# Kernel tuning notes

Hardware: AMD Instinct MI355X
Metric: run time of the kernel (lower is better)

The kernel has to match this reference:

```python
import jax, jax.numpy as jnp
import numpy as np

THRESHOLD = 0.5
ALPHA = 1.0
N, D = 100000, 256
B, K = 1024, 128


def _l2norm(x):
    # F.normalize(x, p=2, dim=-1) with eps=1e-12
    return x / jnp.maximum(jnp.linalg.norm(x, axis=-1, keepdims=True), 1e-12)


def setup_inputs() -> dict:
    key = jax.random.key(0)
    k1, k2, k3, k4, k5, k6, k7 = jax.random.split(key, 7)
    feature = jax.random.normal(k1, (N, D), dtype=jnp.float32)
    text_embedding = jax.random.normal(k2, (N, D), dtype=jnp.float32)
    virtual = jax.random.normal(k3, (1, D), dtype=jnp.float32)
    # Gumbel(0,1) noise for gumbel_softmax (tau=1), materialized for determinism
    u = jax.random.uniform(k4, (B, K, K), dtype=jnp.float32, minval=1e-6, maxval=1.0 - 1e-6)
    gumbel = -jnp.log(-jnp.log(u))
    ego_nodes = jnp.sort(jax.random.randint(k5, (B, K), 0, N, dtype=jnp.int32), axis=-1)
    edges_adj = jax.random.randint(k6, (B, K, K), 0, 2, dtype=jnp.int32)
    train_label = jax.random.randint(k7, (B,), 0, 2, dtype=jnp.int32)
    return {"feature": feature, "text_embedding": text_embedding, "virtual": virtual,
            "gumbel": gumbel, "ego_nodes": ego_nodes, "edges_adj": edges_adj,
            "train_label": train_label}


def reference(feature, text_embedding, virtual, gumbel, ego_nodes, edges_adj, train_label):
    feat = _l2norm(feature)          # self.feature (normalized in __init__)
    emb = _l2norm(text_embedding)    # self.embedding
    te_local = _l2norm(emb - virtual)            # [N, D]

    tb = te_local[ego_nodes]                     # [B, K, D] gather per ego-subgraph
    sim = jnp.einsum('bkd,bjd->bkj', tb, tb) - THRESHOLD   # [B, K, K]
    sim_sub = jax.nn.softmax(sim + gumbel, axis=-1)         # gumbel_softmax, tau=1

    adj = edges_adj.astype(sim_sub.dtype)        # scatter edges_adj[src,dst]=1, precomputed
    # s_diff: row-wise L2 norm then mean over rows
    s_diff = jnp.sqrt(jnp.sum((adj - sim_sub) ** 2, axis=-1)).mean(axis=-1)   # [B]

    emb_out = feat[ego_nodes].mean(axis=1)       # [B, D] sum(feature)/n
    emb_pg = emb[ego_nodes].mean(axis=1)         # [B, D] sum(embedding)/n  (n == K)
    f_diff = jnp.linalg.norm(emb_out - emb_pg, axis=-1)                        # [B]

    score = s_diff + ALPHA * f_diff
    score = (score - score.min()) / (score.max() - score.min())

    y = train_label.astype(score.dtype)
    eps = 1e-7  # stabilizes log at exact 0/1 (torch BCELoss clamps log at -100)
    sc = jnp.clip(score, eps, 1.0 - eps)
    bce = -(y * jnp.log(sc) + (1.0 - y) * jnp.log1p(-sc)).mean()
    loss = bce / y.shape[0]
    return score, loss
```

## Files before the change

kernel.cpp:

```cpp
#include <hip/hip_runtime.h>
#include <math.h>

#define DIM 256
#define BB 1024
#define KK 128
#define PITCH 264

typedef __attribute__((ext_vector_type(8))) short short8;
typedef __attribute__((ext_vector_type(4))) float float4v;

__device__ __forceinline__ unsigned short f2bf(float x) {
    unsigned u = __float_as_uint(x);
    u += 0x7FFFu + ((u >> 16) & 1u);
    return (unsigned short)(u >> 16);
}

__device__ __forceinline__ float dot4(const float4 a, const float4 b) {
    return a.x*b.x + a.y*b.y + a.z*b.z + a.w*b.w;
}

__global__ __launch_bounds__(512, 4) void fused_main(
    const float* __restrict__ feature,
    const float* __restrict__ text,
    const float* __restrict__ virt,
    const float* __restrict__ gumbel,
    const int*   __restrict__ ego,
    const int*   __restrict__ adj,
    float*       __restrict__ score_raw)
{
    __shared__ unsigned short tbs[KK * PITCH];
    __shared__ float fpart[8][DIM];
    __shared__ float spart[8];

    const int b    = blockIdx.x;
    const int tid  = threadIdx.x;
    const int wave = tid >> 6;
    const int lane = tid & 63;

    const float4 vv = ((const float4*)virt)[lane];
    float vv2 = dot4(vv, vv);
    #pragma unroll
    for (int m = 1; m < 64; m <<= 1) vv2 += __shfl_xor(vv2, m);

    const int* ego_b = ego + b * KK;
    const int  base  = wave * 16;

    float fd0 = 0.f, fd1 = 0.f, fd2 = 0.f, fd3 = 0.f;

    int ea = ego_b[base + 0], eb = ego_b[base + 1];
    float4 nta = ((const float4*)(text    + (size_t)ea * DIM))[lane];
    float4 nfa = ((const float4*)(feature + (size_t)ea * DIM))[lane];
    float4 ntb = ((const float4*)(text    + (size_t)eb * DIM))[lane];
    float4 nfb = ((const float4*)(feature + (size_t)eb * DIM))[lane];

    #pragma unroll
    for (int kk = 0; kk < 16; kk += 2) {
        const float4 at = nta, af = nfa, bt = ntb, bf = nfb;
        if (kk + 2 < 16) {
            const int na = ego_b[base + kk + 2], nb = ego_b[base + kk + 3];
            nta = ((const float4*)(text    + (size_t)na * DIM))[lane];
            nfa = ((const float4*)(feature + (size_t)na * DIM))[lane];
            ntb = ((const float4*)(text    + (size_t)nb * DIM))[lane];
            nfb = ((const float4*)(feature + (size_t)nb * DIM))[lane];
        }
        float sta = dot4(at, at), sfa = dot4(af, af), sva = dot4(at, vv);
        float stb = dot4(bt, bt), sfb = dot4(bf, bf), svb = dot4(bt, vv);
        #pragma unroll
        for (int m = 1; m < 64; m <<= 1) {
            sta += __shfl_xor(sta, m);  sfa += __shfl_xor(sfa, m);  sva += __shfl_xor(sva, m);
            stb += __shfl_xor(stb, m);  sfb += __shfl_xor(sfb, m);  svb += __shfl_xor(svb, m);
        }
        {
            const float inv_ne = 1.f / fmaxf(sqrtf(sta), 1e-12f);
            const float inv_nf = 1.f / fmaxf(sqrtf(sfa), 1e-12f);
            const float nw2    = fmaxf(1.f + vv2 - 2.f * sva * inv_ne, 0.f);
            const float inv_nt = 1.f / fmaxf(sqrtf(nw2), 1e-12f);
            const float ex = at.x*inv_ne, ey = at.y*inv_ne, ez = at.z*inv_ne, ew = at.w*inv_ne;
            fd0 += af.x*inv_nf - ex;  fd1 += af.y*inv_nf - ey;
            fd2 += af.z*inv_nf - ez;  fd3 += af.w*inv_nf - ew;
            ushort4 pk;
            pk.x = f2bf((ex - vv.x) * inv_nt);
            pk.y = f2bf((ey - vv.y) * inv_nt);
            pk.z = f2bf((ez - vv.z) * inv_nt);
            pk.w = f2bf((ew - vv.w) * inv_nt);
            *(ushort4*)&tbs[(base + kk) * PITCH + 4 * lane] = pk;
        }
        {
            const float inv_ne = 1.f / fmaxf(sqrtf(stb), 1e-12f);
            const float inv_nf = 1.f / fmaxf(sqrtf(sfb), 1e-12f);
            const float nw2    = fmaxf(1.f + vv2 - 2.f * svb * inv_ne, 0.f);
            const float inv_nt = 1.f / fmaxf(sqrtf(nw2), 1e-12f);
            const float ex = bt.x*inv_ne, ey = bt.y*inv_ne, ez = bt.z*inv_ne, ew = bt.w*inv_ne;
            fd0 += bf.x*inv_nf - ex;  fd1 += bf.y*inv_nf - ey;
            fd2 += bf.z*inv_nf - ez;  fd3 += bf.w*inv_nf - ew;
            ushort4 pk;
            pk.x = f2bf((ex - vv.x) * inv_nt);
            pk.y = f2bf((ey - vv.y) * inv_nt);
            pk.z = f2bf((ez - vv.z) * inv_nt);
            pk.w = f2bf((ew - vv.w) * inv_nt);
            *(ushort4*)&tbs[(base + kk + 1) * PITCH + 4 * lane] = pk;
        }
    }
    fpart[wave][4*lane + 0] = fd0;
    fpart[wave][4*lane + 1] = fd1;
    fpart[wave][4*lane + 2] = fd2;
    fpart[wave][4*lane + 3] = fd3;
    __syncthreads();

    const int g = lane >> 4;
    const int c = lane & 15;

    const float* gb = gumbel + (size_t)b * KK * KK;
    const int*   ab = adj    + (size_t)b * KK * KK;

    float gvv[32];
    #pragma unroll
    for (int r = 0; r < 4; ++r) {
        const float* gr = gb + (base + g*4 + r) * KK + c;
        #pragma unroll
        for (int t = 0; t < 8; ++t)
            gvv[r*8 + t] = __builtin_nontemporal_load(gr + t*16);
    }

    float4v acc[8];
    const float4v zero = {0.f, 0.f, 0.f, 0.f};
    #pragma unroll
    for (int t = 0; t < 8; ++t) acc[t] = zero;

    #pragma unroll
    for (int q = 0; q < 8; ++q) {
        const int dq = q * 32 + g * 8;
        const short8 afr = *(const short8*)&tbs[(base + c) * PITCH + dq];
        #pragma unroll
        for (int t = 0; t < 8; ++t) {
            const short8 bfr = *(const short8*)&tbs[(t*16 + c) * PITCH + dq];
            acc[t] = __builtin_amdgcn_mfma_f32_16x16x32_bf16(afr, bfr, acc[t], 0, 0, 0);
        }
    }

    int avv[32];
    #pragma unroll
    for (int r = 0; r < 4; ++r) {
        const int* ar = ab + (base + g*4 + r) * KK + c;
        #pragma unroll
        for (int t = 0; t < 8; ++t)
            avv[r*8 + t] = __builtin_nontemporal_load(ar + t*16);
    }

    float rs = 0.f;
    #pragma unroll
    for (int r = 0; r < 4; ++r) {
        float s = 0.f, a1 = 0.f, a2 = 0.f, a3 = 0.f;
        #pragma unroll
        for (int t = 0; t < 8; ++t) {
            const float vt = acc[t][r] - 0.5f + gvv[r*8 + t];
            const float et = __expf(vt);
            const float ad = (float)avv[r*8 + t];
            s  += et;
            a3 += et * et;
            a1 += ad;
            a2 += ad * et;
        }
        #pragma unroll
        for (int msk = 1; msk < 16; msk <<= 1) {
            s  += __shfl_xor(s,  msk);
            a1 += __shfl_xor(a1, msk);
            a2 += __shfl_xor(a2, msk);
            a3 += __shfl_xor(a3, msk);
        }
        const float invS = 1.f / s;
        const float T = a1 - 2.f * invS * a2 + invS * invS * a3;
        rs += sqrtf(fmaxf(T, 0.f));
    }
    rs += __shfl_xor(rs, 16);
    rs += __shfl_xor(rs, 32);
    if (lane == 0) spart[wave] = rs;
    __syncthreads();

    if (wave == 0) {
        float d0 = 0.f, d1 = 0.f, d2 = 0.f, d3 = 0.f;
        #pragma unroll
        for (int w = 0; w < 8; ++w) {
            d0 += fpart[w][lane];
            d1 += fpart[w][lane + 64];
            d2 += fpart[w][lane + 128];
            d3 += fpart[w][lane + 192];
        }
        const float inv = 1.f / 128.f;
        d0 *= inv; d1 *= inv; d2 *= inv; d3 *= inv;
        float q2 = d0*d0 + d1*d1 + d2*d2 + d3*d3;
        #pragma unroll
        for (int m = 1; m < 64; m <<= 1) q2 += __shfl_xor(q2, m);
        if (lane == 0) {
            float stot = 0.f;
            #pragma unroll
            for (int w = 0; w < 8; ++w) stot += spart[w];
            score_raw[b] = stot * (1.f / 128.f) + sqrtf(q2);
        }
    }
}

__global__ __launch_bounds__(1024) void finalize(
    const float* __restrict__ score_raw,
    const int*   __restrict__ label,
    float*       __restrict__ out)
{
    __shared__ float wmin[16], wmax[16], wsum[16];
    const int tid = threadIdx.x;
    const float s = score_raw[tid];
    float mn = s, mx = s;
    #pragma unroll
    for (int m = 1; m < 64; m <<= 1) {
        mn = fminf(mn, __shfl_xor(mn, m));
        mx = fmaxf(mx, __shfl_xor(mx, m));
    }
    if ((tid & 63) == 0) { wmin[tid >> 6] = mn; wmax[tid >> 6] = mx; }
    __syncthreads();
    float gmn = wmin[0], gmx = wmax[0];
    #pragma unroll
    for (int w = 1; w < 16; ++w) {
        gmn = fminf(gmn, wmin[w]);
        gmx = fmaxf(gmx, wmax[w]);
    }
    const float score = (s - gmn) / (gmx - gmn);
    out[tid] = score;

    const float y  = (float)label[tid];
    const float sc = fminf(fmaxf(score, 1e-7f), 1.f - 1e-7f);
    float term = -(y * logf(sc) + (1.f - y) * log1pf(-sc));
    #pragma unroll
    for (int m = 1; m < 64; m <<= 1) term += __shfl_xor(term, m);
    if ((tid & 63) == 0) wsum[tid >> 6] = term;
    __syncthreads();
    if (tid == 0) {
        float tot = 0.f;
        #pragma unroll
        for (int w = 0; w < 16; ++w) tot += wsum[w];
        out[BB] = tot / (1024.f * 1024.f);
    }
}

extern "C" void kernel_launch(void* const* d_in, const int* in_sizes, int n_in,
                              void* d_out, int out_size, void* d_ws, size_t ws_size,
                              hipStream_t stream) {
    const float* feature = (const float*)d_in[0];
    const float* text    = (const float*)d_in[1];
    const float* virt    = (const float*)d_in[2];
    const float* gumbel  = (const float*)d_in[3];
    const int*   ego     = (const int*)d_in[4];
    const int*   adj     = (const int*)d_in[5];
    const int*   label   = (const int*)d_in[6];
    float* out       = (float*)d_out;
    float* score_raw = (float*)d_ws;

    fused_main<<<BB, 512, 0, stream>>>(feature, text, virt, gumbel, ego, adj, score_raw);
    finalize<<<1, 1024, 0, stream>>>(score_raw, label, out);
}
```

Measured before the change: 76.09 us.

## Remap gather phase to 16-lane row groups and move gumbel load ahead of barrier

The normalization/gather phase now assigns each quarter-wave (16 lanes) to one node row, with each lane holding 16 floats. This replaces full-wave 64-lane shuffle reductions with 16-lane reductions, processing 4 rows in parallel per iteration. It also uses hardware rsq/rcp intrinsics and packed bf16 conversion, and issues the gumbel loads before the barrier so they overlap the barrier wait. In exchange, register pressure rises and the approximate rsq/rcp may differ slightly in precision from the exact division and sqrt.

```diff
diff --git a/kernel.cpp b/kernel.cpp
--- a/kernel.cpp
+++ b/kernel.cpp
@@ -1,4 +1,5 @@
 #include <hip/hip_runtime.h>
+#include <hip/hip_bf16.h>
 #include <math.h>
 
 #define DIM 256
@@ -9,14 +10,15 @@
 typedef __attribute__((ext_vector_type(8))) short short8;
 typedef __attribute__((ext_vector_type(4))) float float4v;
 
-__device__ __forceinline__ unsigned short f2bf(float x) {
-    unsigned u = __float_as_uint(x);
-    u += 0x7FFFu + ((u >> 16) & 1u);
-    return (unsigned short)(u >> 16);
-}
-
 __device__ __forceinline__ float dot4(const float4 a, const float4 b) {
     return a.x*b.x + a.y*b.y + a.z*b.z + a.w*b.w;
+}
+
+__device__ __forceinline__ unsigned bf2bits(float a, float b) {
+    float2 t; t.x = a; t.y = b;
+    __hip_bfloat162 h = __float22bfloat162_rn(t);
+    unsigned u; __builtin_memcpy(&u, &h, 4);
+    return u;
 }
 
 __global__ __launch_bounds__(512, 4) void fused_main(
@@ -36,83 +38,110 @@
     const int tid  = threadIdx.x;
     const int wave = tid >> 6;
     const int lane = tid & 63;
-
-    const float4 vv = ((const float4*)virt)[lane];
-    float vv2 = dot4(vv, vv);
-    #pragma unroll
-    for (int m = 1; m < 64; m <<= 1) vv2 += __shfl_xor(vv2, m);
+    const int g    = lane >> 4;
+    const int c    = lane & 15;
+
+    float4 vm[4];
+    #pragma unroll
+    for (int m = 0; m < 4; ++m) vm[m] = *(const float4*)(virt + 64*m + 4*c);
+
+    float vv2 = 0.f;
+    #pragma unroll
+    for (int m = 0; m < 4; ++m) vv2 += dot4(vm[m], vm[m]);
+    #pragma unroll
+    for (int msk = 1; msk < 16; msk <<= 1) vv2 += __shfl_xor(vv2, msk);
 
     const int* ego_b = ego + b * KK;
     const int  base  = wave * 16;
 
-    float fd0 = 0.f, fd1 = 0.f, fd2 = 0.f, fd3 = 0.f;
-
-    int ea = ego_b[base + 0], eb = ego_b[base + 1];
-    float4 nta = ((const float4*)(text    + (size_t)ea * DIM))[lane];
-    float4 nfa = ((const float4*)(feature + (size_t)ea * DIM))[lane];
-    float4 ntb = ((const float4*)(text    + (size_t)eb * DIM))[lane];
-    float4 nfb = ((const float4*)(feature + (size_t)eb * DIM))[lane];
-
-    #pragma unroll
-    for (int kk = 0; kk < 16; kk += 2) {
-        const float4 at = nta, af = nfa, bt = ntb, bf = nfb;
-        if (kk + 2 < 16) {
-            const int na = ego_b[base + kk + 2], nb = ego_b[base + kk + 3];
-            nta = ((const float4*)(text    + (size_t)na * DIM))[lane];
-            nfa = ((const float4*)(feature + (size_t)na * DIM))[lane];
-            ntb = ((const float4*)(text    + (size_t)nb * DIM))[lane];
-            nfb = ((const float4*)(feature + (size_t)nb * DIM))[lane];
-        }
-        float sta = dot4(at, at), sfa = dot4(af, af), sva = dot4(at, vv);
-        float stb = dot4(bt, bt), sfb = dot4(bf, bf), svb = dot4(bt, vv);
-        #pragma unroll
-        for (int m = 1; m < 64; m <<= 1) {
-            sta += __shfl_xor(sta, m);  sfa += __shfl_xor(sfa, m);  sva += __shfl_xor(sva, m);
-            stb += __shfl_xor(stb, m);  sfb += __shfl_xor(sfb, m);  svb += __shfl_xor(svb, m);
-        }
-        {
-            const float inv_ne = 1.f / fmaxf(sqrtf(sta), 1e-12f);
-            const float inv_nf = 1.f / fmaxf(sqrtf(sfa), 1e-12f);
-            const float nw2    = fmaxf(1.f + vv2 - 2.f * sva * inv_ne, 0.f);
-            const float inv_nt = 1.f / fmaxf(sqrtf(nw2), 1e-12f);
-            const float ex = at.x*inv_ne, ey = at.y*inv_ne, ez = at.z*inv_ne, ew = at.w*inv_ne;
-            fd0 += af.x*inv_nf - ex;  fd1 += af.y*inv_nf - ey;
-            fd2 += af.z*inv_nf - ez;  fd3 += af.w*inv_nf - ew;
-            ushort4 pk;
-            pk.x = f2bf((ex - vv.x) * inv_nt);
-            pk.y = f2bf((ey - vv.y) * inv_nt);
-            pk.z = f2bf((ez - vv.z) * inv_nt);
-            pk.w = f2bf((ew - vv.w) * inv_nt);
-            *(ushort4*)&tbs[(base + kk) * PITCH + 4 * lane] = pk;
-        }
-        {
-            const float inv_ne = 1.f / fmaxf(sqrtf(stb), 1e-12f);
-            const float inv_nf = 1.f / fmaxf(sqrtf(sfb), 1e-12f);
-            const float nw2    = fmaxf(1.f + vv2 - 2.f * svb * inv_ne, 0.f);
-            const float inv_nt = 1.f / fmaxf(sqrtf(nw2), 1e-12f);
-            const float ex = bt.x*inv_ne, ey = bt.y*inv_ne, ez = bt.z*inv_ne, ew = bt.w*inv_ne;
-            fd0 += bf.x*inv_nf - ex;  fd1 += bf.y*inv_nf - ey;
-            fd2 += bf.z*inv_nf - ez;  fd3 += bf.w*inv_nf - ew;
-            ushort4 pk;
-            pk.x = f2bf((ex - vv.x) * inv_nt);
-            pk.y = f2bf((ey - vv.y) * inv_nt);
-            pk.z = f2bf((ez - vv.z) * inv_nt);
-            pk.w = f2bf((ew - vv.w) * inv_nt);
-            *(ushort4*)&tbs[(base + kk + 1) * PITCH + 4 * lane] = pk;
-        }
-    }
-    fpart[wave][4*lane + 0] = fd0;
-    fpart[wave][4*lane + 1] = fd1;
-    fpart[wave][4*lane + 2] = fd2;
-    fpart[wave][4*lane + 3] = fd3;
-    __syncthreads();
-
-    const int g = lane >> 4;
-    const int c = lane & 15;
+    int eidx[4];
+    #pragma unroll
+    for (int it = 0; it < 4; ++it) eidx[it] = ego_b[base + it*4 + g];
+
+    float4 fd[4];
+    #pragma unroll
+    for (int m = 0; m < 4; ++m) fd[m] = make_float4(0.f, 0.f, 0.f, 0.f);
+
+    float4 nt[4], nf[4];
+    {
+        const float* tr = text    + (size_t)eidx[0] * DIM + 4*c;
+        const float* fr = feature + (size_t)eidx[0] * DIM + 4*c;
+        #pragma unroll
+        for (int m = 0; m < 4; ++m) {
+            nt[m] = *(const float4*)(tr + 64*m);
+            nf[m] = *(const float4*)(fr + 64*m);
+        }
+    }
+
+    #pragma unroll
+    for (int it = 0; it < 4; ++it) {
+        float4 ct[4], cf[4];
+        #pragma unroll
+        for (int m = 0; m < 4; ++m) { ct[m] = nt[m]; cf[m] = nf[m]; }
+        if (it < 3) {
+            const float* tr = text    + (size_t)eidx[it+1] * DIM + 4*c;
+            const float* fr = feature + (size_t)eidx[it+1] * DIM + 4*c;
+            #pragma unroll
+            for (int m = 0; m < 4; ++m) {
+                nt[m] = *(const float4*)(tr + 64*m);
+                nf[m] = *(const float4*)(fr + 64*m);
+            }
+        }
+
+        float st = 0.f, sf = 0.f, sv = 0.f;
+        #pragma unroll
+        for (int m = 0; m < 4; ++m) {
+            st += dot4(ct[m], ct[m]);
+            sf += dot4(cf[m], cf[m]);
+            sv += dot4(ct[m], vm[m]);
+        }
+        #pragma unroll
+        for (int msk = 1; msk < 16; msk <<= 1) {
+            st += __shfl_xor(st, msk);
+            sf += __shfl_xor(sf, msk);
+            sv += __shfl_xor(sv, msk);
+        }
+
+        const float inv_ne = __builtin_amdgcn_rsqf(fmaxf(st, 1e-24f));
+        const float inv_nf = __builtin_amdgcn_rsqf(fmaxf(sf, 1e-24f));
+        const float nw2    = fmaxf(1.f + vv2 - 2.f * sv * inv_ne, 1e-24f);
+        const float inv_nt = __builtin_amdgcn_rsqf(nw2);
+
+        const int row = base + it*4 + g;
+        unsigned short* dst = &tbs[row * PITCH + 4*c];
+        #pragma unroll
+        for (int m = 0; m < 4; ++m) {
+            const float e0 = ct[m].x * inv_ne, e1 = ct[m].y * inv_ne;
+            const float e2 = ct[m].z * inv_ne, e3 = ct[m].w * inv_ne;
+            fd[m].x += cf[m].x * inv_nf - e0;
+            fd[m].y += cf[m].y * inv_nf - e1;
+            fd[m].z += cf[m].z * inv_nf - e2;
+            fd[m].w += cf[m].w * inv_nf - e3;
+            uint2 pk;
+            pk.x = bf2bits((e0 - vm[m].x) * inv_nt, (e1 - vm[m].y) * inv_nt);
+            pk.y = bf2bits((e2 - vm[m].z) * inv_nt, (e3 - vm[m].w) * inv_nt);
+            *(uint2*)(dst + 64*m) = pk;
+        }
+    }
+
+    #pragma unroll
+    for (int msk = 16; msk < 64; msk <<= 1) {
+        #pragma unroll
+        for (int m = 0; m < 4; ++m) {
+            fd[m].x += __shfl_xor(fd[m].x, msk);
+            fd[m].y += __shfl_xor(fd[m].y, msk);
+            fd[m].z += __shfl_xor(fd[m].z, msk);
+            fd[m].w += __shfl_xor(fd[m].w, msk);
+        }
+    }
+    if (g == 0) {
+        #pragma unroll
+        for (int m = 0; m < 4; ++m)
+            *(float4*)&fpart[wave][64*m + 4*c] = fd[m];
+    }
 
     const float* gb = gumbel + (size_t)b * KK * KK;
     const int*   ab = adj    + (size_t)b * KK * KK;
-
     float gvv[32];
     #pragma unroll
     for (int r = 0; r < 4; ++r) {
@@ -121,6 +150,8 @@
         for (int t = 0; t < 8; ++t)
             gvv[r*8 + t] = __builtin_nontemporal_load(gr + t*16);
     }
+
+    __syncthreads();
 
     float4v acc[8];
     const float4v zero = {0.f, 0.f, 0.f, 0.f};
@@ -150,26 +181,27 @@
     float rs = 0.f;
     #pragma unroll
     for (int r = 0; r < 4; ++r) {
-        float s = 0.f, a1 = 0.f, a2 = 0.f, a3 = 0.f;
+        float s = 0.f, a2 = 0.f, a3 = 0.f;
+        int   ia = 0;
         #pragma unroll
         for (int t = 0; t < 8; ++t) {
             const float vt = acc[t][r] - 0.5f + gvv[r*8 + t];
             const float et = __expf(vt);
-            const float ad = (float)avv[r*8 + t];
+            const int   ad = avv[r*8 + t];
             s  += et;
             a3 += et * et;
-            a1 += ad;
-            a2 += ad * et;
+            ia += ad;
+            a2 += ad ? et : 0.f;
         }
         #pragma unroll
         for (int msk = 1; msk < 16; msk <<= 1) {
             s  += __shfl_xor(s,  msk);
-            a1 += __shfl_xor(a1, msk);
             a2 += __shfl_xor(a2, msk);
             a3 += __shfl_xor(a3, msk);
-        }
-        const float invS = 1.f / s;
-        const float T = a1 - 2.f * invS * a2 + invS * invS * a3;
+            ia += __shfl_xor(ia, msk);
+        }
+        const float invS = __builtin_amdgcn_rcpf(s);
+        const float T = (float)ia - invS * (2.f * a2 - invS * a3);
         rs += sqrtf(fmaxf(T, 0.f));
     }
     rs += __shfl_xor(rs, 16);
```

Measured after the change: 81.06 us. +6.5%, slower.
